# Kernel tuning notes

Hardware: AMD Instinct MI355X
Metric: run time of the kernel (lower is better)

The kernel has to match this reference:

```python
import jax, jax.numpy as jnp
import numpy as np

DIM = 20
N = 200000
E = 6400000
ITERATIONS = 3


def setup_inputs() -> dict:
    key = jax.random.key(0)
    ks = jax.random.split(key, 20)
    inp = {
        "h": jax.random.normal(ks[0], (N, DIM), dtype=jnp.float32),
        "node2depth": jax.random.randint(ks[1], (N,), 0, 5, dtype=jnp.int32),
        "edge_src": jax.random.randint(ks[2], (E,), 0, N, dtype=jnp.int32),
        "edge_dst": jax.random.randint(ks[3], (E,), 0, N, dtype=jnp.int32),
    }
    # Six DIM x DIM Linear layers (weight stored [out,in] like torch, plus bias)
    scale = 1.0 / np.sqrt(DIM)
    names = ["Wz", "Uz", "Wr", "Ur", "Wh", "Uh"]
    for j, nm in enumerate(names):
        inp[nm + "_w"] = jax.random.uniform(ks[4 + 2 * j], (DIM, DIM), jnp.float32, -scale, scale)
        inp[nm + "_b"] = jax.random.uniform(ks[5 + 2 * j], (DIM,), jnp.float32, -scale, scale)
    return inp


def _linear(x, w, b):
    return x @ w.T + b


def reference(h, Wz_w, Wz_b, Uz_w, Uz_b, Wr_w, Wr_b, Ur_w, Ur_b,
              Wh_w, Wh_b, Uh_w, Uh_b, node2depth, edge_src, edge_dst):
    active = None
    for i in range(ITERATIONS):
        # active set shrinks as i grows (depth + i <= ITERATIONS)
        active = (node2depth + i) <= ITERATIONS  # [N] bool
        af = active.astype(h.dtype)
        # x[u] = sum over neighbors v of h[v], counting only active src AND active dst
        msg = h[edge_src] * af[edge_src][:, None]          # [E, DIM]
        x = jax.ops.segment_sum(msg, edge_dst, num_segments=N)  # [N, DIM]
        x = x * af[:, None]
        z = jax.nn.sigmoid(_linear(x, Wz_w, Wz_b) + _linear(h, Uz_w, Uz_b))
        r = jax.nn.sigmoid(_linear(x, Wr_w, Wr_b) + _linear(h, Ur_w, Ur_b))
        h_cand = jnp.tanh(_linear(x, Wh_w, Wh_b) + _linear(r * h, Uh_w, Uh_b))
        h_new = z * h + (1.0 - z) * h_cand
        # inactive nodes are dropped from the dict in the original; since the
        # active set only shrinks, keeping their old h is equivalent
        h = jnp.where(active[:, None], h_new, h)
    # original returns only nodes active at the last iteration; zero out the rest
    return jnp.where(active[:, None], h, jnp.zeros_like(h))
```

## Files before the change

### kernel.cpp

```cpp
#include <hip/hip_runtime.h>

#define DIM    20
#define NN     200000
#define EE     6400000
#define ITERS  3
#define BLOCK  256

#define NODES_PER_FINE   64
#define NFINE            3125
#define NCOARSE          98
#define FINE_PER_COARSE  32

#define TILE1            2048
#define IPT1             8

#define TILE             4096
#define IPT              16

#define CAP1             57344
#define NT2P             14
#define CAP2             2048
#define PQ               2

typedef unsigned int u32;

__global__ void init_cursors(int* __restrict__ coarse_cursor,
                             int* __restrict__ fine_cursor,
                             int* __restrict__ gcur) {
    int g = blockIdx.x * 256 + threadIdx.x;
    if (g < NCOARSE) coarse_cursor[g] = g * CAP1;
    if (g < NFINE)   fine_cursor[g]   = g * CAP2;
    if (g == 0) *gcur = 0;
}

__global__ __launch_bounds__(BLOCK) void kdep(const int* __restrict__ depth,
                                              int* __restrict__ dcnt) {
    __shared__ u32 dh[5];
    int tid = threadIdx.x;
    if (tid < 5) dh[tid] = 0;
    __syncthreads();
    for (int n = blockIdx.x * BLOCK + tid; n < NN; n += gridDim.x * BLOCK)
        atomicAdd(&dh[depth[n]], 1u);
    __syncthreads();
    if (tid < 5) dcnt[tid * 256 + blockIdx.x] = (int)dh[tid];
}

__global__ __launch_bounds__(BLOCK) void k2_scan(const int* __restrict__ dcnt,
                                                 int* __restrict__ dbase,
                                                 int* __restrict__ cum) {
    __shared__ int wsum[4];
    __shared__ int sdb[1281];
    int tid = threadIdx.x;
    int lane = tid & 63, wid = tid >> 6;
    const int CH2 = 5;
    int loc[CH2];
    int base = tid * CH2;
    int s = 0;
    #pragma unroll
    for (int j = 0; j < CH2; ++j) { int v = dcnt[base + j]; loc[j] = v; s += v; }
    int incl = s;
    #pragma unroll
    for (int off = 1; off < 64; off <<= 1) {
        int t = __shfl_up(incl, off, 64);
        if (lane >= off) incl += t;
    }
    if (lane == 63) wsum[wid] = incl;
    __syncthreads();
    int woff = 0;
    for (int w = 0; w < wid; ++w) woff += wsum[w];
    int run = woff + incl - s;
    #pragma unroll
    for (int j = 0; j < CH2; ++j) {
        sdb[base + j]   = run;
        dbase[base + j] = run;
        run += loc[j];
    }
    if (tid == 255) sdb[1280] = run;
    __syncthreads();
    if (tid < 5) cum[tid] = sdb[(tid + 1) * 256];
}

__global__ __launch_bounds__(BLOCK) void kd_scatter(const int* __restrict__ depth,
                                                    const int* __restrict__ dbase,
                                                    int* __restrict__ perm) {
    __shared__ u32 dh[5];
    int tid = threadIdx.x;
    if (tid < 5) dh[tid] = 0;
    __syncthreads();
    for (int n = blockIdx.x * BLOCK + tid; n < NN; n += gridDim.x * BLOCK) {
        int d = depth[n];
        u32 r = atomicAdd(&dh[d], 1u);
        perm[n] = dbase[d * 256 + blockIdx.x] + (int)r;
    }
}

__global__ __launch_bounds__(BLOCK) void p1_split(const int* __restrict__ esrc,
                                                  const int* __restrict__ edst,
                                                  const int* __restrict__ perm,
                                                  const int* __restrict__ cum,
                                                  int* __restrict__ coarse_cursor,
                                                  u32* __restrict__ buf1) {
    __shared__ u32 lhist[NCOARSE];
    __shared__ u32 gbase[NCOARSE];
    int tid = threadIdx.x;
    int start = blockIdx.x * TILE1;
    if (tid < NCOARSE) lhist[tid] = 0;
    __syncthreads();
    const u32 c3 = (u32)cum[3];

    int4 d4[2], s4[2];
    #pragma unroll
    for (int q = 0; q < 2; ++q) {
        int e4 = start + (q * BLOCK + tid) * 4;
        d4[q] = *(const int4*)(edst + e4);
        s4[q] = *(const int4*)(esrc + e4);
    }
    u32 pid[IPT1];
    #pragma unroll
    for (int q = 0; q < 2; ++q) {
        pid[q * 4 + 0] = (u32)perm[s4[q].x];
        pid[q * 4 + 1] = (u32)perm[s4[q].y];
        pid[q * 4 + 2] = (u32)perm[s4[q].z];
        pid[q * 4 + 3] = (u32)perm[s4[q].w];
    }
    int dd[IPT1];
    #pragma unroll
    for (int q = 0; q < 2; ++q) {
        dd[q * 4 + 0] = d4[q].x; dd[q * 4 + 1] = d4[q].y;
        dd[q * 4 + 2] = d4[q].z; dd[q * 4 + 3] = d4[q].w;
    }
    u32 key[IPT1], rank[IPT1];
    #pragma unroll
    for (int k = 0; k < IPT1; ++k) {
        key[k] = 0xFFFFu;
        if (pid[k] < c3) {
            key[k]  = (u32)dd[k] >> 11;
            rank[k] = atomicAdd(&lhist[key[k]], 1u);
        }
    }
    __syncthreads();
    if (tid < NCOARSE) {
        u32 c = lhist[tid];
        gbase[tid] = c ? (u32)atomicAdd((u32*)&coarse_cursor[tid], c) : 0u;
    }
    __syncthreads();
    #pragma unroll
    for (int k = 0; k < IPT1; ++k) {
        if (key[k] != 0xFFFFu)
            buf1[gbase[key[k]] + rank[k]] = ((u32)dd[k] & 2047u) | (pid[k] << 11);
    }
}

__global__ __launch_bounds__(BLOCK) void p2_split(const u32* __restrict__ buf1,
                                                  const int* __restrict__ coarse_cursor,
                                                  int* __restrict__ fine_cursor,
                                                  u32* __restrict__ buf2) {
    int bid = blockIdx.x;
    int c = bid / NT2P, t = bid - c * NT2P;
    int base  = c * CAP1;
    int end   = coarse_cursor[c];
    int start = base + t * TILE;
    if (start >= end) return;

    __shared__ u32 lhist[FINE_PER_COARSE];
    __shared__ u32 gbase[FINE_PER_COARSE];
    int tid = threadIdx.x;
    if (tid < FINE_PER_COARSE) lhist[tid] = 0;
    __syncthreads();

    u32 w[IPT];
    #pragma unroll
    for (int q = 0; q < 4; ++q) {
        int i4 = start + (q * BLOCK + tid) * 4;
        if (i4 + 3 < end) {
            uint4 v = *(const uint4*)(buf1 + i4);
            w[q * 4 + 0] = v.x; w[q * 4 + 1] = v.y;
            w[q * 4 + 2] = v.z; w[q * 4 + 3] = v.w;
        } else {
            #pragma unroll
            for (int j = 0; j < 4; ++j) {
                int i = i4 + j;
                w[q * 4 + j] = (i < end) ? buf1[i] : 0xFFFFFFFFu;
            }
        }
    }
    u32 key[IPT], rank[IPT];
    #pragma unroll
    for (int k = 0; k < IPT; ++k) {
        if (w[k] != 0xFFFFFFFFu) {
            key[k]  = (w[k] & 2047u) >> 6;
            rank[k] = atomicAdd(&lhist[key[k]], 1u);
        }
    }
    __syncthreads();
    if (tid < FINE_PER_COARSE) {
        u32 cnt = lhist[tid];
        int f = c * FINE_PER_COARSE + tid;
        if (cnt && f < NFINE)
            gbase[tid] = (u32)atomicAdd((u32*)&fine_cursor[f], cnt);
    }
    __syncthreads();
    #pragma unroll
    for (int k = 0; k < IPT; ++k) {
        if (w[k] != 0xFFFFFFFFu)
            buf2[gbase[key[k]] + rank[k]] = (w[k] & 63u) | ((w[k] >> 11) << 6);
    }
}

__global__ __launch_bounds__(BLOCK) void pb_sort(const u32* __restrict__ buf2,
                                                 const int* __restrict__ fine_cursor,
                                                 const int* __restrict__ cum,
                                                 int* __restrict__ gcur,
                                                 int* __restrict__ ptr,
                                                 u32* __restrict__ cnt3,
                                                 u32* __restrict__ ssrc) {
    __shared__ u32 hist[512];
    __shared__ u32 ebase[512];
    __shared__ u32 lout[CAP2];
    __shared__ u32 wsum[4];
    __shared__ int slo;
    int tid = threadIdx.x;
    int f = blockIdx.x;
    int base = f * CAP2;
    int end  = fine_cursor[f];
    int cnt  = end - base;
    u32 c0 = (u32)cum[0], c1 = (u32)cum[1], c2 = (u32)cum[2], c3 = (u32)cum[3];
    hist[tid] = 0; hist[tid + 256] = 0;
    __syncthreads();

    u32 w[PQ * 4];
    #pragma unroll
    for (int q = 0; q < PQ; ++q) {
        int i4 = base + (q * BLOCK + tid) * 4;
        if (i4 + 3 < end) {
            uint4 v = *(const uint4*)(buf2 + i4);
            w[q * 4 + 0] = v.x; w[q * 4 + 1] = v.y;
            w[q * 4 + 2] = v.z; w[q * 4 + 3] = v.w;
        } else {
            #pragma unroll
            for (int j = 0; j < 4; ++j) {
                int i = i4 + j;
                w[q * 4 + j] = (i < end) ? buf2[i] : 0xFFFFFFFFu;
            }
        }
    }
    u32 key[PQ * 4], rank[PQ * 4];
    #pragma unroll
    for (int k = 0; k < PQ * 4; ++k) {
        if (w[k] != 0xFFFFFFFFu) {
            u32 pid = w[k] >> 6;
            u32 dep = (u32)(pid >= c0) + (u32)(pid >= c1)
                    + (u32)(pid >= c2) + (u32)(pid >= c3);
            key[k]  = (w[k] & 63u) * 8u + dep;
            rank[k] = atomicAdd(&hist[key[k]], 1u);
        }
    }
    if (tid == 0) slo = atomicAdd(gcur, cnt);
    __syncthreads();
    {
        u32 s0 = hist[2 * tid], s1 = hist[2 * tid + 1];
        u32 s = s0 + s1;
        int lane = tid & 63, wid = tid >> 6;
        u32 incl = s;
        #pragma unroll
        for (int off = 1; off < 64; off <<= 1) {
            u32 t = __shfl_up((int)incl, off, 64);
            if (lane >= off) incl += t;
        }
        if (lane == 63) wsum[wid] = incl;
        __syncthreads();
        u32 woff = 0;
        for (int w2 = 0; w2 < wid; ++w2) woff += wsum[w2];
        u32 excl = woff + incl - s;
        ebase[2 * tid]     = excl;
        ebase[2 * tid + 1] = excl + s0;
    }
    __syncthreads();
    int lo = slo;
    if (tid < NODES_PER_FINE) {
        u32 base0 = ebase[tid * 8];
        u32 cc1 = ebase[tid * 8 + 2] - base0;
        u32 cc2 = ebase[tid * 8 + 3] - base0;
        u32 cc3 = ebase[tid * 8 + 4] - base0;
        int u = f * NODES_PER_FINE + tid;
        ptr[u]  = lo + (int)base0;
        cnt3[u] = cc1 | (cc2 << 10) | (cc3 << 20);
    }
    #pragma unroll
    for (int k = 0; k < PQ * 4; ++k) {
        if (w[k] != 0xFFFFFFFFu) lout[ebase[key[k]] + rank[k]] = w[k] >> 6;
    }
    __syncthreads();
    for (int j = tid; j < cnt; j += BLOCK) ssrc[lo + j] = lout[j];
}

__device__ __forceinline__ u32 pack_bf16x2(float a, float b) {
    u32 ua = __float_as_uint(a);
    u32 ub = __float_as_uint(b);
    ua = (ua + 0x7FFFu + ((ua >> 16) & 1u)) >> 16;
    ub = (ub + 0x7FFFu + ((ub >> 16) & 1u)) & 0xFFFF0000u;
    return ua | ub;
}

__global__ __launch_bounds__(BLOCK) void hconv(const float* __restrict__ h,
                                               u32* __restrict__ hbA,
                                               u32* __restrict__ hbC,
                                               const int* __restrict__ perm,
                                               const int* __restrict__ depth) {
    int g = blockIdx.x * BLOCK + threadIdx.x;
    if (g >= NN * 8) return;
    int node = g >> 3, s = g & 7;
    if (depth[node] > ITERS) return;
    int pid = perm[node];
    float2 f = *(const float2*)(h + (size_t)node * DIM + s * 2);
    hbA[(size_t)pid * 8 + s] = pack_bf16x2(f.x, f.y);
    if (s < 2) {
        float2 fc = *(const float2*)(h + (size_t)node * DIM + 16 + s * 2);
        hbC[(size_t)pid * 2 + s] = pack_bf16x2(fc.x, fc.y);
    }
}


__device__ __forceinline__ float bl(u32 w) { return __uint_as_float(w << 16); }
__device__ __forceinline__ float bh(u32 w) { return __uint_as_float(w & 0xFFFF0000u); }

__device__ __forceinline__ void acc_half(float* xa, float* xc, uint4 a, u32 c) {
    xa[0]+=bl(a.x); xa[1]+=bh(a.x);
    xa[2]+=bl(a.y); xa[3]+=bh(a.y);
    xa[4]+=bl(a.z); xa[5]+=bh(a.z);
    xa[6]+=bl(a.w); xa[7]+=bh(a.w);
    xc[0]+=bl(c);   xc[1]+=bh(c);
}

__global__ __launch_bounds__(BLOCK) void gather_x(
    const u32* __restrict__ hbA, const u32* __restrict__ hbC,
    const int* __restrict__ depth, const int* __restrict__ ptr,
    const u32* __restrict__ cnt3, const u32* __restrict__ ssrc,
    float* __restrict__ xg, int lim, int shift)
{
    int tid = threadIdx.x;
    int u = blockIdx.x * 32 + (tid >> 3);
    int j = tid & 7;
    int r = j >> 1;
    int q = j & 1;
    if (depth[u] > lim) return;
    int p = ptr[u];
    int d = (int)((cnt3[u] >> shift) & 1023u);

    float xa[8], xc[2];
    #pragma unroll
    for (int k = 0; k < 8; ++k) xa[k] = 0.0f;
    xc[0] = 0.0f; xc[1] = 0.0f;

    int e = r;
    for (; e + 12 < d; e += 16) {
        u32 p0 = ssrc[p + e];
        u32 p1 = ssrc[p + e + 4];
        u32 p2 = ssrc[p + e + 8];
        u32 p3 = ssrc[p + e + 12];
        uint4 a0 = *(const uint4*)(hbA + (size_t)p0 * 8 + q * 4);
        uint4 a1 = *(const uint4*)(hbA + (size_t)p1 * 8 + q * 4);
        uint4 a2 = *(const uint4*)(hbA + (size_t)p2 * 8 + q * 4);
        uint4 a3 = *(const uint4*)(hbA + (size_t)p3 * 8 + q * 4);
        u32 c0 = hbC[(size_t)p0 * 2 + q];
        u32 c1 = hbC[(size_t)p1 * 2 + q];
        u32 c2 = hbC[(size_t)p2 * 2 + q];
        u32 c3 = hbC[(size_t)p3 * 2 + q];
        acc_half(xa, xc, a0, c0);
        acc_half(xa, xc, a1, c1);
        acc_half(xa, xc, a2, c2);
        acc_half(xa, xc, a3, c3);
    }
    for (; e + 4 < d; e += 8) {
        u32 p0 = ssrc[p + e];
        u32 p1 = ssrc[p + e + 4];
        uint4 a0 = *(const uint4*)(hbA + (size_t)p0 * 8 + q * 4);
        uint4 a1 = *(const uint4*)(hbA + (size_t)p1 * 8 + q * 4);
        u32 c0 = hbC[(size_t)p0 * 2 + q];
        u32 c1 = hbC[(size_t)p1 * 2 + q];
        acc_half(xa, xc, a0, c0);
        acc_half(xa, xc, a1, c1);
    }
    if (e < d) {
        u32 p0 = ssrc[p + e];
        uint4 a0 = *(const uint4*)(hbA + (size_t)p0 * 8 + q * 4);
        u32 c0 = hbC[(size_t)p0 * 2 + q];
        acc_half(xa, xc, a0, c0);
    }
    #pragma unroll
    for (int k = 0; k < 8; ++k) {
        xa[k] += __shfl_xor(xa[k], 2, 64);
        xa[k] += __shfl_xor(xa[k], 4, 64);
    }
    xc[0] += __shfl_xor(xc[0], 2, 64); xc[0] += __shfl_xor(xc[0], 4, 64);
    xc[1] += __shfl_xor(xc[1], 2, 64); xc[1] += __shfl_xor(xc[1], 4, 64);

    float* xr = xg + (size_t)u * DIM;
    if (j == 0) {
        *(float4*)(xr)      = make_float4(xa[0], xa[1], xa[2], xa[3]);
        *(float4*)(xr + 4)  = make_float4(xa[4], xa[5], xa[6], xa[7]);
        *(float2*)(xr + 16) = make_float2(xc[0], xc[1]);
    } else if (j == 1) {
        *(float4*)(xr + 8)  = make_float4(xa[0], xa[1], xa[2], xa[3]);
        *(float4*)(xr + 12) = make_float4(xa[4], xa[5], xa[6], xa[7]);
        *(float2*)(xr + 18) = make_float2(xc[0], xc[1]);
    }
}


__device__ __forceinline__ float fast_sigmoid(float t) {
    return 1.0f / (1.0f + __expf(-t));
}
__device__ __forceinline__ float fast_tanh(float t) {
    t = fminf(fmaxf(t, -15.0f), 15.0f);
    float e2 = __expf(2.0f * t);
    return (e2 - 1.0f) / (e2 + 1.0f);
}

__global__ __launch_bounds__(BLOCK) void gru_update(
    const float* __restrict__ xg,
    const float* __restrict__ h_in, float* __restrict__ h_out,
    u32* __restrict__ hbA, u32* __restrict__ hbC,
    const int* __restrict__ depth, const int* __restrict__ perm,
    const int* __restrict__ cum,
    const float* __restrict__ Wz, const float* __restrict__ bWz,
    const float* __restrict__ Uz, const float* __restrict__ bUz,
    const float* __restrict__ Wr, const float* __restrict__ bWr,
    const float* __restrict__ Ur, const float* __restrict__ bUr,
    const float* __restrict__ Wh, const float* __restrict__ bWh,
    const float* __restrict__ Uh, const float* __restrict__ bUh,
    int lim, int cumIdx, int isFinal)
{
    int u = blockIdx.x * BLOCK + threadIdx.x;
    if (u >= NN) return;
    bool act = depth[u] <= lim;
    if (!act) {
        if (isFinal) {
            float4 z4 = make_float4(0.f, 0.f, 0.f, 0.f);
            float4* o4 = (float4*)(h_out + (size_t)u * DIM);
            #pragma unroll
            for (int q = 0; q < 5; ++q) o4[q] = z4;
        }
        return;
    }

    float x[DIM], h[DIM];
    {
        const float4* xv = (const float4*)(xg + (size_t)u * DIM);
        float4 a0 = xv[0], a1 = xv[1], a2 = xv[2], a3 = xv[3], a4 = xv[4];
        x[0]=a0.x; x[1]=a0.y; x[2]=a0.z; x[3]=a0.w;
        x[4]=a1.x; x[5]=a1.y; x[6]=a1.z; x[7]=a1.w;
        x[8]=a2.x; x[9]=a2.y; x[10]=a2.z; x[11]=a2.w;
        x[12]=a3.x; x[13]=a3.y; x[14]=a3.z; x[15]=a3.w;
        x[16]=a4.x; x[17]=a4.y; x[18]=a4.z; x[19]=a4.w;
    }
    {
        const float4* hv = (const float4*)(h_in + (size_t)u * DIM);
        float4 a0 = hv[0], a1 = hv[1], a2 = hv[2], a3 = hv[3], a4 = hv[4];
        h[0]=a0.x; h[1]=a0.y; h[2]=a0.z; h[3]=a0.w;
        h[4]=a1.x; h[5]=a1.y; h[6]=a1.z; h[7]=a1.w;
        h[8]=a2.x; h[9]=a2.y; h[10]=a2.z; h[11]=a2.w;
        h[12]=a3.x; h[13]=a3.y; h[14]=a3.z; h[15]=a3.w;
        h[16]=a4.x; h[17]=a4.y; h[18]=a4.z; h[19]=a4.w;
    }

    float z[DIM], rh[DIM];
    #pragma unroll
    for (int j = 0; j < DIM; ++j) {
        float sz = bWz[j] + bUz[j];
        float sr = bWr[j] + bUr[j];
        #pragma unroll
        for (int k = 0; k < DIM; ++k) {
            sz += x[k] * Wz[j * DIM + k];
            sz += h[k] * Uz[j * DIM + k];
            sr += x[k] * Wr[j * DIM + k];
            sr += h[k] * Ur[j * DIM + k];
        }
        z[j]  = fast_sigmoid(sz);
        rh[j] = fast_sigmoid(sr) * h[j];
    }

    float o[DIM];
    #pragma unroll
    for (int j = 0; j < DIM; ++j) {
        float sh = bWh[j] + bUh[j];
        #pragma unroll
        for (int k = 0; k < DIM; ++k) {
            sh += x[k]  * Wh[j * DIM + k];
            sh += rh[k] * Uh[j * DIM + k];
        }
        float hc = fast_tanh(sh);
        o[j] = z[j] * h[j] + (1.0f - z[j]) * hc;
    }

    {
        float4* o4 = (float4*)(h_out + (size_t)u * DIM);
        o4[0] = make_float4(o[0],  o[1],  o[2],  o[3]);
        o4[1] = make_float4(o[4],  o[5],  o[6],  o[7]);
        o4[2] = make_float4(o[8],  o[9],  o[10], o[11]);
        o4[3] = make_float4(o[12], o[13], o[14], o[15]);
        o4[4] = make_float4(o[16], o[17], o[18], o[19]);
    }
    if (!isFinal) {
        int pid = perm[u];
        if (pid < cum[cumIdx]) {
            u32* rowA = hbA + (size_t)pid * 8;
            uint4 wA0 = make_uint4(pack_bf16x2(o[0], o[1]),   pack_bf16x2(o[2], o[3]),
                                   pack_bf16x2(o[4], o[5]),   pack_bf16x2(o[6], o[7]));
            uint4 wA1 = make_uint4(pack_bf16x2(o[8], o[9]),   pack_bf16x2(o[10], o[11]),
                                   pack_bf16x2(o[12], o[13]), pack_bf16x2(o[14], o[15]));
            *(uint4*)rowA       = wA0;
            *(uint4*)(rowA + 4) = wA1;
            *(uint2*)(hbC + (size_t)pid * 2) =
                make_uint2(pack_bf16x2(o[16], o[17]), pack_bf16x2(o[18], o[19]));
        }
    }
}


extern "C" void kernel_launch(void* const* d_in, const int* in_sizes, int n_in,
                              void* d_out, int out_size, void* d_ws, size_t ws_size,
                              hipStream_t stream) {
    const float* h0    = (const float*)d_in[0];
    const int*   depth = (const int*)d_in[1];
    const int*   esrc  = (const int*)d_in[2];
    const int*   edst  = (const int*)d_in[3];
    const float* Wz  = (const float*)d_in[4];  const float* bWz = (const float*)d_in[5];
    const float* Uz  = (const float*)d_in[6];  const float* bUz = (const float*)d_in[7];
    const float* Wr  = (const float*)d_in[8];  const float* bWr = (const float*)d_in[9];
    const float* Ur  = (const float*)d_in[10]; const float* bUr = (const float*)d_in[11];
    const float* Wh  = (const float*)d_in[12]; const float* bWh = (const float*)d_in[13];
    const float* Uh  = (const float*)d_in[14]; const float* bUh = (const float*)d_in[15];
    float* out = (float*)d_out;

    int* W = (int*)d_ws;
    int*  dcnt          = W + 0;
    int*  dbase         = W + 1280;
    int*  cum           = W + 2560;
    int*  gcur          = W + 2568;
    int*  coarse_cursor = W + 2576;
    int*  fine_cursor   = W + 2688;
    int*  ptr           = W + 5824;
    u32*  cnt3          = (u32*)(W + 205824);
    int*  perm          = W + 405824;
    u32*  buf1          = (u32*)(W + 605824);
    u32*  buf2          = buf1 + (size_t)NCOARSE * CAP1;
    float* h1           = (float*)(buf2 + (size_t)NFINE * CAP2);
    u32*  hbA           = (u32*)(h1 + (size_t)NN * DIM);
    u32*  hbC           = hbA + (size_t)NN * 8;
    u32*  ssrc          = buf1;
    float* xg           = (float*)buf2;

    init_cursors<<<13, 256, 0, stream>>>(coarse_cursor, fine_cursor, gcur);
    kdep        <<<256, BLOCK, 0, stream>>>(depth, dcnt);
    k2_scan     <<<1,   BLOCK, 0, stream>>>(dcnt, dbase, cum);
    kd_scatter  <<<256, BLOCK, 0, stream>>>(depth, dbase, perm);
    p1_split    <<<EE / TILE1, BLOCK, 0, stream>>>(esrc, edst, perm, cum, coarse_cursor, buf1);
    p2_split    <<<NCOARSE * NT2P, BLOCK, 0, stream>>>(buf1, coarse_cursor, fine_cursor, buf2);
    pb_sort     <<<NFINE, BLOCK, 0, stream>>>(buf2, fine_cursor, cum, gcur, ptr, cnt3, ssrc);
    hconv       <<<(NN * 8) / BLOCK, BLOCK, 0, stream>>>(h0, hbA, hbC, perm, depth);

    gather_x  <<<NN / 32, BLOCK, 0, stream>>>(hbA, hbC, depth, ptr, cnt3, ssrc, xg, 3, 20);
    gru_update<<<(NN + BLOCK - 1) / BLOCK, BLOCK, 0, stream>>>(xg, h0, h1, hbA, hbC, depth, perm, cum,
        Wz, bWz, Uz, bUz, Wr, bWr, Ur, bUr, Wh, bWh, Uh, bUh, 3, 2, 0);
    gather_x  <<<NN / 32, BLOCK, 0, stream>>>(hbA, hbC, depth, ptr, cnt3, ssrc, xg, 2, 10);
    gru_update<<<(NN + BLOCK - 1) / BLOCK, BLOCK, 0, stream>>>(xg, h1, h1, hbA, hbC, depth, perm, cum,
        Wz, bWz, Uz, bUz, Wr, bWr, Ur, bUr, Wh, bWh, Uh, bUh, 2, 1, 0);
    gather_x  <<<NN / 32, BLOCK, 0, stream>>>(hbA, hbC, depth, ptr, cnt3, ssrc, xg, 1, 0);
    gru_update<<<(NN + BLOCK - 1) / BLOCK, BLOCK, 0, stream>>>(xg, h1, out, hbA, hbC, depth, perm, cum,
        Wz, bWz, Uz, bUz, Wr, bWr, Ur, bUr, Wh, bWh, Uh, bUh, 1, 0, 1);
}
```

Baseline: 526.5 us.

## Stage partition scatter through shared memory for coalesced bucket writes

Both radix-partition passes now compute a per-tile exclusive prefix over bucket counts with wavefront shuffles. Each pass writes its elements into a shared-memory staging buffer ordered by bucket, then copies each bucket out contiguously with one wavefront per bucket. This replaces scattered per-element global stores with coalesced runs, aiming to reduce write transactions. The cost is extra LDS (up to 16KB per block), an additional barrier and scan step, and possibly lower occupancy.

```diff
diff --git a/kernel.cpp b/kernel.cpp
--- a/kernel.cpp
+++ b/kernel.cpp
@@ -100,11 +100,13 @@
                                                   const int* __restrict__ cum,
                                                   int* __restrict__ coarse_cursor,
                                                   u32* __restrict__ buf1) {
-    __shared__ u32 lhist[NCOARSE];
+    __shared__ u32 hist[NCOARSE];
+    __shared__ u32 lbase[NCOARSE];
     __shared__ u32 gbase[NCOARSE];
+    __shared__ u32 lout[TILE1];
     int tid = threadIdx.x;
     int start = blockIdx.x * TILE1;
-    if (tid < NCOARSE) lhist[tid] = 0;
+    if (tid < NCOARSE) hist[tid] = 0;
     __syncthreads();
     const u32 c3 = (u32)cum[3];
 
@@ -116,38 +118,51 @@
         s4[q] = *(const int4*)(esrc + e4);
     }
     u32 pid[IPT1];
-    #pragma unroll
-    for (int q = 0; q < 2; ++q) {
-        pid[q * 4 + 0] = (u32)perm[s4[q].x];
-        pid[q * 4 + 1] = (u32)perm[s4[q].y];
-        pid[q * 4 + 2] = (u32)perm[s4[q].z];
-        pid[q * 4 + 3] = (u32)perm[s4[q].w];
-    }
+    pid[0] = (u32)perm[s4[0].x]; pid[1] = (u32)perm[s4[0].y];
+    pid[2] = (u32)perm[s4[0].z]; pid[3] = (u32)perm[s4[0].w];
+    pid[4] = (u32)perm[s4[1].x]; pid[5] = (u32)perm[s4[1].y];
+    pid[6] = (u32)perm[s4[1].z]; pid[7] = (u32)perm[s4[1].w];
+    asm volatile("" :: "v"(pid[0]), "v"(pid[1]), "v"(pid[2]), "v"(pid[3]),
+                       "v"(pid[4]), "v"(pid[5]), "v"(pid[6]), "v"(pid[7]));
     int dd[IPT1];
-    #pragma unroll
-    for (int q = 0; q < 2; ++q) {
-        dd[q * 4 + 0] = d4[q].x; dd[q * 4 + 1] = d4[q].y;
-        dd[q * 4 + 2] = d4[q].z; dd[q * 4 + 3] = d4[q].w;
-    }
-    u32 key[IPT1], rank[IPT1];
-    #pragma unroll
-    for (int k = 0; k < IPT1; ++k) {
-        key[k] = 0xFFFFu;
-        if (pid[k] < c3) {
-            key[k]  = (u32)dd[k] >> 11;
-            rank[k] = atomicAdd(&lhist[key[k]], 1u);
-        }
+    dd[0]=d4[0].x; dd[1]=d4[0].y; dd[2]=d4[0].z; dd[3]=d4[0].w;
+    dd[4]=d4[1].x; dd[5]=d4[1].y; dd[6]=d4[1].z; dd[7]=d4[1].w;
+
+    u32 rank[IPT1];
+    #pragma unroll
+    for (int k = 0; k < IPT1; ++k)
+        if (pid[k] < c3) rank[k] = atomicAdd(&hist[(u32)dd[k] >> 11], 1u);
+    __syncthreads();
+
+    if (tid < 64) {
+        u32 a = hist[tid];
+        u32 b = (tid + 64 < NCOARSE) ? hist[tid + 64] : 0u;
+        u32 ia = a, ib = b;
+        #pragma unroll
+        for (int off = 1; off < 64; off <<= 1) {
+            u32 ta = (u32)__shfl_up((int)ia, off, 64);
+            u32 tb = (u32)__shfl_up((int)ib, off, 64);
+            if (tid >= off) { ia += ta; ib += tb; }
+        }
+        u32 totA = (u32)__shfl((int)ia, 63, 64);
+        lbase[tid] = ia - a;
+        if (tid + 64 < NCOARSE) lbase[tid + 64] = totA + ib - b;
     }
     __syncthreads();
     if (tid < NCOARSE) {
-        u32 c = lhist[tid];
-        gbase[tid] = c ? (u32)atomicAdd((u32*)&coarse_cursor[tid], c) : 0u;
-    }
-    __syncthreads();
-    #pragma unroll
-    for (int k = 0; k < IPT1; ++k) {
-        if (key[k] != 0xFFFFu)
-            buf1[gbase[key[k]] + rank[k]] = ((u32)dd[k] & 2047u) | (pid[k] << 11);
+        u32 cq = hist[tid];
+        gbase[tid] = cq ? (u32)atomicAdd((u32*)&coarse_cursor[tid], cq) : 0u;
+    }
+    #pragma unroll
+    for (int k = 0; k < IPT1; ++k)
+        if (pid[k] < c3)
+            lout[lbase[(u32)dd[k] >> 11] + rank[k]] = ((u32)dd[k] & 2047u) | (pid[k] << 11);
+    __syncthreads();
+    int wid = tid >> 6, lane = tid & 63;
+    for (int b = wid; b < NCOARSE; b += 4) {
+        u32 cq = hist[b], lb = lbase[b], gb = gbase[b];
+        for (u32 i = lane; i < cq; i += 64)
+            buf1[gb + i] = lout[lb + i];
     }
 }
 
@@ -162,10 +177,12 @@
     int start = base + t * TILE;
     if (start >= end) return;
 
-    __shared__ u32 lhist[FINE_PER_COARSE];
+    __shared__ u32 hist[FINE_PER_COARSE];
+    __shared__ u32 lbase[FINE_PER_COARSE];
     __shared__ u32 gbase[FINE_PER_COARSE];
-    int tid = threadIdx.x;
-    if (tid < FINE_PER_COARSE) lhist[tid] = 0;
+    __shared__ u32 lout[TILE];
+    int tid = threadIdx.x;
+    if (tid < FINE_PER_COARSE) hist[tid] = 0;
     __syncthreads();
 
     u32 w[IPT];
@@ -184,26 +201,35 @@
             }
         }
     }
-    u32 key[IPT], rank[IPT];
-    #pragma unroll
-    for (int k = 0; k < IPT; ++k) {
-        if (w[k] != 0xFFFFFFFFu) {
-            key[k]  = (w[k] & 2047u) >> 6;
-            rank[k] = atomicAdd(&lhist[key[k]], 1u);
-        }
-    }
-    __syncthreads();
-    if (tid < FINE_PER_COARSE) {
-        u32 cnt = lhist[tid];
+    u32 rank[IPT];
+    #pragma unroll
+    for (int k = 0; k < IPT; ++k)
+        if (w[k] != 0xFFFFFFFFu)
+            rank[k] = atomicAdd(&hist[(w[k] & 2047u) >> 6], 1u);
+    __syncthreads();
+
+    if (tid < 32) {
+        u32 a = hist[tid], ia = a;
+        #pragma unroll
+        for (int off = 1; off < 32; off <<= 1) {
+            u32 ta = (u32)__shfl_up((int)ia, off, 32);
+            if (tid >= off) ia += ta;
+        }
+        lbase[tid] = ia - a;
         int f = c * FINE_PER_COARSE + tid;
-        if (cnt && f < NFINE)
-            gbase[tid] = (u32)atomicAdd((u32*)&fine_cursor[f], cnt);
-    }
-    __syncthreads();
-    #pragma unroll
-    for (int k = 0; k < IPT; ++k) {
+        gbase[tid] = a ? (u32)atomicAdd((u32*)&fine_cursor[f], a) : 0u;
+    }
+    __syncthreads();
+    #pragma unroll
+    for (int k = 0; k < IPT; ++k)
         if (w[k] != 0xFFFFFFFFu)
-            buf2[gbase[key[k]] + rank[k]] = (w[k] & 63u) | ((w[k] >> 11) << 6);
+            lout[lbase[(w[k] & 2047u) >> 6] + rank[k]] = (w[k] & 63u) | ((w[k] >> 11) << 6);
+    __syncthreads();
+    int wid = tid >> 6, lane = tid & 63;
+    for (int b = wid; b < FINE_PER_COARSE; b += 4) {
+        u32 cq = hist[b], lb = lbase[b], gb = gbase[b];
+        for (u32 i = lane; i < cq; i += 64)
+            buf2[gb + i] = lout[lb + i];
     }
 }
 
```

New measurement: 524.0 us. About the same (-0.5%).
